# Optimization experiments

Measured on AMD Instinct MI355X. Metric: run time of the kernel, lower is better.

Reference implementation:

```python
import jax, jax.numpy as jnp
import numpy as np

K = 3
K2 = K * K
STRIDE, PAD, DIL = 1, 1, 1


def conv2d(x, w, b, stride, pad, dil):
    out = jax.lax.conv_general_dilated(
        x, w, (stride, stride), [(pad, pad), (pad, pad)],
        rhs_dilation=(dil, dil),
        dimension_numbers=("NCHW", "OIHW", "NCHW"))
    return out + b[None, :, None, None]


def deform_sample(img, py, px):
    """Bilinear sample with zero padding outside.
    img: [C,H,W]; py,px: [K2,Ho,Wo] float sample coords -> [C,K2,Ho,Wo]."""
    C, H, W = img.shape
    y0 = jnp.floor(py)
    x0 = jnp.floor(px)
    acc = jnp.zeros((C,) + py.shape, img.dtype)
    for dy in (0.0, 1.0):
        for dx in (0.0, 1.0):
            yi = y0 + dy
            xi = x0 + dx
            wgt = (1.0 - jnp.abs(py - yi)) * (1.0 - jnp.abs(px - xi))
            valid = (yi >= 0) & (yi < H) & (xi >= 0) & (xi < W)
            yc = jnp.clip(yi, 0, H - 1).astype(jnp.int32)
            xc = jnp.clip(xi, 0, W - 1).astype(jnp.int32)
            v = img[:, yc, xc]  # gather -> [C,K2,Ho,Wo]
            acc = acc + v * (wgt * valid)[None]
    return acc


def setup_inputs() -> dict:
    key = jax.random.key(0)
    k1, k2, k3, k4 = jax.random.split(key, 4)
    Cin, Cout = 64, 64
    x = jax.random.normal(k1, (4, Cin, 128, 128), jnp.float32)
    # small offset-conv weights so learned offsets stay in a few-pixel range
    w_off = jax.random.normal(k2, (3 * K2, Cin, K, K), jnp.float32) * 0.01
    b_off = jnp.zeros((3 * K2,), jnp.float32)
    # folded (BN-fused) deform conv weight/bias
    w = jax.random.normal(k3, (Cout, Cin, K, K), jnp.float32) * (1.0 / np.sqrt(Cin * K2))
    b = jax.random.normal(k4, (Cout,), jnp.float32) * 0.1
    return {"x": x, "w_off": w_off, "b_off": b_off, "w": w, "b": b}


def reference(x, w_off, b_off, w, b):
    N, C, H, W = x.shape
    # offset/mask conv -> chunk into (o1, o2, mask), cat offsets, sigmoid mask
    om = conv2d(x, w_off, b_off, STRIDE, PAD, DIL)  # [N, 27, Ho, Wo]
    o1, o2, m = jnp.split(om, 3, axis=1)
    offset = jnp.concatenate([o1, o2], axis=1)      # [N, 2*K2, Ho, Wo]
    mask = jax.nn.sigmoid(m)                        # [N, K2, Ho, Wo]
    Ho, Wo = offset.shape[2], offset.shape[3]
    # torchvision layout: per kernel tap (dy, dx) pairs
    off = offset.reshape(N, K2, 2, Ho, Wo)
    dy, dx = off[:, :, 0], off[:, :, 1]
    hk, wk = jnp.meshgrid(jnp.arange(K), jnp.arange(K), indexing="ij")
    base_y = ((jnp.arange(Ho) * STRIDE - PAD)[None, :, None]
              + (hk.reshape(K2) * DIL)[:, None, None])  # [K2,Ho,1]
    base_x = ((jnp.arange(Wo) * STRIDE - PAD)[None, None, :]
              + (wk.reshape(K2) * DIL)[:, None, None])  # [K2,1,Wo]
    py = base_y.astype(x.dtype) + dy                    # [N,K2,Ho,Wo]
    px = base_x.astype(x.dtype) + dx
    sampled = jax.vmap(deform_sample)(x, py, px)        # [N,C,K2,Ho,Wo]
    sampled = sampled * mask[:, None]
    out = jnp.einsum("ock,nckhw->nohw", w.reshape(w.shape[0], C, K2), sampled)
    out = out + b[None, :, None, None]
    return jax.nn.relu(out)
```

## Files before the change

kernel.cpp:

```cpp
#include <hip/hip_runtime.h>
#include <math.h>

#define N_ 4
#define C_ 64
#define H_ 128
#define W_ 128
#define HW_ (H_ * W_)
#define K2_ 9
#define COUT 64
#define CK 576
#define TP 16
#define NT 2
#define SST 584
#define GUARD 128
#define DEPTH 6
#define SLOTS 7

typedef __bf16 bf16x8 __attribute__((ext_vector_type(8)));
typedef __bf16 bf16x2 __attribute__((ext_vector_type(2)));
typedef float floatx4 __attribute__((ext_vector_type(4)));
typedef float floatx2 __attribute__((ext_vector_type(2)));
typedef unsigned uint2v __attribute__((ext_vector_type(2)));

__device__ __forceinline__ float bflo(unsigned u) {
    return __builtin_bit_cast(float, u << 16);
}
__device__ __forceinline__ float bfhi(unsigned u) {
    return __builtin_bit_cast(float, u & 0xffff0000u);
}

__global__ __launch_bounds__(256) void prep_kernel(const float* __restrict__ x,
                                                   const float* __restrict__ w,
                                                   const float* __restrict__ w_off,
                                                   __bf16* __restrict__ xT,
                                                   __bf16* __restrict__ w2,
                                                   __bf16* __restrict__ w_off2) {
    __shared__ float s_t[64][33];
    int t = threadIdx.x;
    int bx = blockIdx.x;
    int y = blockIdx.y, n = blockIdx.z;
    if (bx < 4) {
        int x0 = bx * 32;
        int c = t >> 2, seg = (t & 3) * 8;
        const float* src = x + (((size_t)n * C_ + c) * H_ + y) * W_ + x0 + seg;
        floatx4 v0 = *(const floatx4*)src;
        floatx4 v1 = *(const floatx4*)(src + 4);
#pragma unroll
        for (int j = 0; j < 4; ++j) { s_t[c][seg + j] = v0[j]; s_t[c][seg + 4 + j] = v1[j]; }
        __syncthreads();
        int xl = t >> 3, cb = (t & 7) * 8;
        bf16x8 o;
#pragma unroll
        for (int j = 0; j < 8; ++j) o[j] = (__bf16)s_t[cb + j][xl];
        *(bf16x8*)(xT + (((size_t)n * H_ + y) * W_ + x0 + xl) * C_ + cb) = o;
    } else {
        int linear = (n * 128 + y) * 256 + t;
        if (linear < COUT * CK) {
            int o = linear / CK, r = linear - o * CK;
            int k = r >> 6, c = r & 63;
            w2[linear] = (__bf16)w[(o * C_ + c) * K2_ + k];
        }
        if (linear < 32 * CK) {
            int o = linear / CK, r = linear - o * CK;
            int k = r >> 6, c = r & 63;
            w_off2[linear] = (o < 27) ? (__bf16)w_off[(o * C_ + c) * K2_ + k] : (__bf16)0.f;
        }
    }
}

__global__ __launch_bounds__(256) void fused_kernel(const __bf16* __restrict__ xT,
                                                    const __bf16* __restrict__ w2,
                                                    const __bf16* __restrict__ w_off2,
                                                    const float* __restrict__ b_off,
                                                    const float* __restrict__ b,
                                                    float* __restrict__ out) {
    __shared__ __align__(16) __bf16 s_x[NT][TP * SST];
    __shared__ float s_om[NT][2][32 * TP];
    __shared__ floatx4 s_w4[NT][K2_ * TP];
    __shared__ int s_pix[NT][K2_ * TP];

    int t = threadIdx.x;
    int pixbase = blockIdx.x * (TP * NT);
    int wo0 = pixbase & (W_ - 1);
    int ho  = (pixbase >> 7) & (H_ - 1);
    int n   = pixbase >> 14;
    const __bf16* xn = xT + (size_t)n * HW_ * C_;

    int lane = t & 63;
    int wv   = t >> 6;
    int half = lane >> 5;
    int li   = lane & 31;
    int q    = lane >> 4;
    int col  = lane & 15;

    {
        uint2v ua[18];
        int tl = wv >> 1;
        int rb = (wv & 1) * 36 + half;
#pragma unroll
        for (int j = 0; j < 18; ++j) {
            int r  = rb + 2 * j;
            int k  = r >> 3;
            int p0 = (r & 7) * 2;
            int kh = k / 3, kw = k - kh * 3;
            int y  = ho - 1 + kh;
            int yc = min(max(y, 0), H_ - 1);
            int xx = wo0 + 16 * tl + p0 - 1 + kw;
            int pix = yc * W_ + xx;
            ua[j] = *((const uint2v*)(xn + (ptrdiff_t)pix * C_) + li);
        }
#pragma unroll
        for (int j = 0; j < 18; ++j) {
            int r  = rb + 2 * j;
            int k  = r >> 3;
            int p0 = (r & 7) * 2;
            int kh = k / 3, kw = k - kh * 3;
            int y  = ho - 1 + kh;
            int xx = wo0 + 16 * tl + p0 - 1 + kw;
            bool vy = (unsigned)y < (unsigned)H_;
            int myxx = xx + (li >> 4);
            bool valid = vy && ((unsigned)myxx < (unsigned)W_);
            uint2v v = ua[j];
            v.x = valid ? v.x : 0u;
            v.y = valid ? v.y : 0u;
            int p = p0 + (li >> 4);
            *(uint2v*)&s_x[tl][p * SST + k * 64 + 4 * (li & 15)] = v;
        }
    }
    __syncthreads();

    {
        int r = wv >> 1;
        int h = wv & 1;
        const __bf16* ar = w_off2 + (size_t)(16 * r + col) * CK + h * 288 + q * 8;
        const __bf16* b0 = s_x[0] + col * SST + h * 288 + q * 8;
        const __bf16* b1 = s_x[1] + col * SST + h * 288 + q * 8;
        floatx4 acc0 = {0.f, 0.f, 0.f, 0.f}, acc1 = {0.f, 0.f, 0.f, 0.f};
#pragma unroll
        for (int it = 0; it < 9; ++it) {
            bf16x8 a   = *(const bf16x8*)(ar + 32 * it);
            bf16x8 bb0 = *(const bf16x8*)(b0 + 32 * it);
            bf16x8 bb1 = *(const bf16x8*)(b1 + 32 * it);
            acc0 = __builtin_amdgcn_mfma_f32_16x16x32_bf16(a, bb0, acc0, 0, 0, 0);
            acc1 = __builtin_amdgcn_mfma_f32_16x16x32_bf16(a, bb1, acc1, 0, 0, 0);
        }
#pragma unroll
        for (int rr = 0; rr < 4; ++rr) {
            s_om[0][h][(16 * r + q * 4 + rr) * TP + col] = acc0[rr];
            s_om[1][h][(16 * r + q * 4 + rr) * TP + col] = acc1[rr];
        }
    }
    __syncthreads();

#pragma unroll
    for (int it2 = 0; it2 < 2; ++it2) {
        int i = it2 * 256 + t;
        if (i < NT * K2_ * TP) {
            int tl = (i >= 144);
            int P  = i - 144 * tl;
            int k  = P >> 4;
            int pp = P & 15;
            float dy = s_om[tl][0][(2 * k) * TP + pp]     + s_om[tl][1][(2 * k) * TP + pp]     + b_off[2 * k];
            float dx = s_om[tl][0][(2 * k + 1) * TP + pp] + s_om[tl][1][(2 * k + 1) * TP + pp] + b_off[2 * k + 1];
            float mm = s_om[tl][0][(18 + k) * TP + pp]    + s_om[tl][1][(18 + k) * TP + pp]    + b_off[18 + k];
            float msk = 1.f / (1.f + expf(-mm));
            int kh = k / 3, kw = k - kh * 3;
            float py = (float)(ho - 1 + kh) + dy;
            float px = (float)(wo0 + 16 * tl + pp - 1 + kw) + dx;
            float yf = floorf(py), xf = floorf(px);
            float fy = py - yf, fx = px - xf;
            int y0 = (int)yf, x0 = (int)xf;
            float wy0 = ((unsigned)y0 < (unsigned)H_)       ? 1.f - fy : 0.f;
            float wy1 = ((unsigned)(y0 + 1) < (unsigned)H_) ? fy       : 0.f;
            float wx0 = ((unsigned)x0 < (unsigned)W_)       ? 1.f - fx : 0.f;
            float wx1 = ((unsigned)(x0 + 1) < (unsigned)W_) ? fx      : 0.f;
            int y0c = min(max(y0, 0), H_ - 2);
            int x0c = min(max(x0, 0), W_ - 2);
            float t0 = (y0 == y0c) ? wy0 : ((y0 + 1 == y0c) ? wy1 : 0.f);
            float t1 = (y0 == y0c) ? wy1 : ((y0 == y0c + 1) ? wy0 : 0.f);
            float u0 = (x0 == x0c) ? wx0 : ((x0 + 1 == x0c) ? wx1 : 0.f);
            float u1 = (x0 == x0c) ? wx1 : ((x0 == x0c + 1) ? wx0 : 0.f);
            floatx4 w4 = { t0 * u0 * msk, t0 * u1 * msk, t1 * u0 * msk, t1 * u1 * msk };
            s_w4[tl][P] = w4;
            s_pix[tl][P] = y0c * W_ + x0c;
        }
    }
    __syncthreads();

    {
        int Pb = wv * 36 + half;
        int pixv[36];
#pragma unroll
        for (int i = 0; i < 36; ++i) {
            int tl_ = (i >= 18);
            pixv[i] = s_pix[tl_][Pb + 2 * (i - 18 * tl_)];
        }
        unsigned buf[SLOTS][4];

#define ISSUE(gi)                                                                  \
        do {                                                                       \
            const __bf16* a0 = xn + (ptrdiff_t)pixv[(gi)] * C_ + 2 * li;           \
            const __bf16* a1 = a0 + W_ * C_;                                       \
            asm volatile("global_load_dword %0, %4, off\n\t"                       \
                         "global_load_dword %1, %4, off offset:128\n\t"            \
                         "global_load_dword %2, %5, off\n\t"                       \
                         "global_load_dword %3, %5, off offset:128"                \
                         : "=&v"(buf[(gi) % SLOTS][0]), "=&v"(buf[(gi) % SLOTS][1]),\
                           "=&v"(buf[(gi) % SLOTS][2]), "=&v"(buf[(gi) % SLOTS][3])\
                         : "v"(a0), "v"(a1));                                      \
        } while (0)

#define STEP(g, NW)                                                                \
        do {                                                                       \
            if ((g) + DEPTH < 36) ISSUE((g) + DEPTH);                              \
            int tl_ = ((g) >= 18);                                                 \
            int P_  = Pb + 2 * ((g) - 18 * tl_);                                   \
            floatx4 w4_ = s_w4[tl_][P_];                                           \
            asm volatile("s_waitcnt vmcnt(" #NW ")" ::: "memory");                 \
            __builtin_amdgcn_sched_barrier(0);                                     \
            float lo = w4_[0] * bflo(buf[(g) % SLOTS][0])                          \
                     + w4_[1] * bflo(buf[(g) % SLOTS][1])                          \
                     + w4_[2] * bflo(buf[(g) % SLOTS][2])                          \
                     + w4_[3] * bflo(buf[(g) % SLOTS][3]);                         \
            float hi = w4_[0] * bfhi(buf[(g) % SLOTS][0])                          \
                     + w4_[1] * bfhi(buf[(g) % SLOTS][1])                          \
                     + w4_[2] * bfhi(buf[(g) % SLOTS][2])                          \
                     + w4_[3] * bfhi(buf[(g) % SLOTS][3]);                         \
            floatx2 fv = {lo, hi};                                                 \
            bf16x2 bv = __builtin_convertvector(fv, bf16x2);                       \
            int k_ = P_ >> 4, p_ = P_ & 15;                                        \
            *(unsigned*)&s_x[tl_][p_ * SST + k_ * 64 + 2 * li] =                   \
                __builtin_bit_cast(unsigned, bv);                                  \
        } while (0)

        ISSUE(0); ISSUE(1); ISSUE(2); ISSUE(3); ISSUE(4); ISSUE(5);
        STEP(0, 24);  STEP(1, 24);  STEP(2, 24);  STEP(3, 24);  STEP(4, 24);
        STEP(5, 24);  STEP(6, 24);  STEP(7, 24);  STEP(8, 24);  STEP(9, 24);
        STEP(10, 24); STEP(11, 24); STEP(12, 24); STEP(13, 24); STEP(14, 24);
        STEP(15, 24); STEP(16, 24); STEP(17, 24); STEP(18, 24); STEP(19, 24);
        STEP(20, 24); STEP(21, 24); STEP(22, 24); STEP(23, 24); STEP(24, 24);
        STEP(25, 24); STEP(26, 24); STEP(27, 24); STEP(28, 24); STEP(29, 24);
        STEP(30, 20); STEP(31, 16); STEP(32, 12); STEP(33, 8);  STEP(34, 4);
        STEP(35, 0);
#undef STEP
#undef ISSUE
    }
    __syncthreads();

    {
        const __bf16* ar = w2 + (size_t)(16 * wv + col) * CK + q * 8;
        const __bf16* b0 = s_x[0] + col * SST + q * 8;
        const __bf16* b1 = s_x[1] + col * SST + q * 8;
        floatx4 acc0 = {0.f, 0.f, 0.f, 0.f}, acc1 = {0.f, 0.f, 0.f, 0.f};
        bf16x8 a_cur = *(const bf16x8*)ar;
#pragma unroll
        for (int it = 0; it < 18; ++it) {
            bf16x8 a_nxt;
            if (it < 17) a_nxt = *(const bf16x8*)(ar + 32 * (it + 1));
            bf16x8 bb0 = *(const bf16x8*)(b0 + 32 * it);
            bf16x8 bb1 = *(const bf16x8*)(b1 + 32 * it);
            acc0 = __builtin_amdgcn_mfma_f32_16x16x32_bf16(a_cur, bb0, acc0, 0, 0, 0);
            acc1 = __builtin_amdgcn_mfma_f32_16x16x32_bf16(a_cur, bb1, acc1, 0, 0, 0);
            a_cur = a_nxt;
        }
#pragma unroll
        for (int r = 0; r < 4; ++r) {
            int o = 16 * wv + q * 4 + r;
            float bias = b[o];
            float* ob = out + (((size_t)n * COUT + o) * H_ + ho) * W_ + wo0;
            ob[col]      = fmaxf(acc0[r] + bias, 0.f);
            ob[16 + col] = fmaxf(acc1[r] + bias, 0.f);
        }
    }
}

extern "C" void kernel_launch(void* const* d_in, const int* in_sizes, int n_in,
                              void* d_out, int out_size, void* d_ws, size_t ws_size,
                              hipStream_t stream) {
    const float* x     = (const float*)d_in[0];
    const float* w_off = (const float*)d_in[1];
    const float* b_off = (const float*)d_in[2];
    const float* w     = (const float*)d_in[3];
    const float* b     = (const float*)d_in[4];
    float* out = (float*)d_out;

    __bf16* xT     = (__bf16*)d_ws + GUARD;
    __bf16* w2     = xT + (size_t)N_ * HW_ * C_ + GUARD;
    __bf16* w_off2 = w2 + (size_t)COUT * CK;

    prep_kernel<<<dim3(5, 128, 4), 256, 0, stream>>>(x, w, w_off, xT, w2, w_off2);

    int nblocks = N_ * H_ * W_ / (TP * NT);
    fused_kernel<<<nblocks, 256, 0, stream>>>(xT, w2, w_off2, b_off, b, out);
}
```

Baseline: 119.8 us.

## Stage halo rows once in LDS instead of a replicated im2col tile for offset conv

The offset-conv input staging is replaced. Instead of building a 9x-replicated im2col tile per pixel, it loads 3 input rows by 34 pixels by 64 channels as 16-byte vectors into shared memory. The MFMA loop then indexes taps through row and column offsets. This cuts global loads, from 18 narrow loads per thread to 4 wide ones, and cuts LDS writes. The cost is a compile-time branch on h, and padded pixel strides chosen to limit bank conflicts.

```diff
diff --git a/kernel.cpp b/kernel.cpp
--- a/kernel.cpp
+++ b/kernel.cpp
@@ -15,12 +15,15 @@
 #define GUARD 128
 #define DEPTH 6
 #define SLOTS 7
+#define PXS 68
+#define RS  (34 * PXS)
 
 typedef __bf16 bf16x8 __attribute__((ext_vector_type(8)));
 typedef __bf16 bf16x2 __attribute__((ext_vector_type(2)));
 typedef float floatx4 __attribute__((ext_vector_type(4)));
 typedef float floatx2 __attribute__((ext_vector_type(2)));
 typedef unsigned uint2v __attribute__((ext_vector_type(2)));
+typedef unsigned uint4v __attribute__((ext_vector_type(4)));
 
 __device__ __forceinline__ float bflo(unsigned u) {
     return __builtin_bit_cast(float, u << 16);
@@ -78,6 +81,7 @@
     __shared__ float s_om[NT][2][32 * TP];
     __shared__ floatx4 s_w4[NT][K2_ * TP];
     __shared__ int s_pix[NT][K2_ * TP];
+    __bf16* s_row = &s_x[0][0];
 
     int t = threadIdx.x;
     int pixbase = blockIdx.x * (TP * NT);
@@ -94,37 +98,33 @@
     int col  = lane & 15;
 
     {
-        uint2v ua[18];
-        int tl = wv >> 1;
-        int rb = (wv & 1) * 36 + half;
-#pragma unroll
-        for (int j = 0; j < 18; ++j) {
-            int r  = rb + 2 * j;
-            int k  = r >> 3;
-            int p0 = (r & 7) * 2;
-            int kh = k / 3, kw = k - kh * 3;
-            int y  = ho - 1 + kh;
+        uint4v va[4];
+#pragma unroll
+        for (int it = 0; it < 4; ++it) {
+            int i  = it * 256 + t;
+            int s  = i & 7;
+            int pr = i >> 3;
+            int r  = pr / 34;
+            int p  = pr - r * 34;
+            int y  = ho - 1 + r;
             int yc = min(max(y, 0), H_ - 1);
-            int xx = wo0 + 16 * tl + p0 - 1 + kw;
-            int pix = yc * W_ + xx;
-            ua[j] = *((const uint2v*)(xn + (ptrdiff_t)pix * C_) + li);
-        }
-#pragma unroll
-        for (int j = 0; j < 18; ++j) {
-            int r  = rb + 2 * j;
-            int k  = r >> 3;
-            int p0 = (r & 7) * 2;
-            int kh = k / 3, kw = k - kh * 3;
-            int y  = ho - 1 + kh;
-            int xx = wo0 + 16 * tl + p0 - 1 + kw;
-            bool vy = (unsigned)y < (unsigned)H_;
-            int myxx = xx + (li >> 4);
-            bool valid = vy && ((unsigned)myxx < (unsigned)W_);
-            uint2v v = ua[j];
-            v.x = valid ? v.x : 0u;
-            v.y = valid ? v.y : 0u;
-            int p = p0 + (li >> 4);
-            *(uint2v*)&s_x[tl][p * SST + k * 64 + 4 * (li & 15)] = v;
+            int x  = wo0 - 1 + p;
+            const __bf16* ap = xn + (ptrdiff_t)(yc * W_ + x) * C_ + s * 8;
+            va[it] = *(const uint4v*)ap;
+        }
+#pragma unroll
+        for (int it = 0; it < 4; ++it) {
+            int i  = it * 256 + t;
+            int s  = i & 7;
+            int pr = i >> 3;
+            int r  = pr / 34;
+            int p  = pr - r * 34;
+            int y  = ho - 1 + r;
+            int x  = wo0 - 1 + p;
+            bool valid = ((unsigned)y < (unsigned)H_) && ((unsigned)x < (unsigned)W_);
+            uint4v v = va[it];
+            if (!valid) v = (uint4v){0u, 0u, 0u, 0u};
+            if (i < 3 * 34 * 8) *(uint4v*)&s_row[r * RS + p * PXS + s * 8] = v;
         }
     }
     __syncthreads();
@@ -132,18 +132,31 @@
     {
         int r = wv >> 1;
         int h = wv & 1;
-        const __bf16* ar = w_off2 + (size_t)(16 * r + col) * CK + h * 288 + q * 8;
-        const __bf16* b0 = s_x[0] + col * SST + h * 288 + q * 8;
-        const __bf16* b1 = s_x[1] + col * SST + h * 288 + q * 8;
+        const __bf16* ar  = w_off2 + (size_t)(16 * r + col) * CK + h * 288 + q * 8;
+        const __bf16* rb0 = s_row + col * PXS + q * 8;
+        const __bf16* rb1 = rb0 + 16 * PXS;
         floatx4 acc0 = {0.f, 0.f, 0.f, 0.f}, acc1 = {0.f, 0.f, 0.f, 0.f};
-#pragma unroll
-        for (int it = 0; it < 9; ++it) {
-            bf16x8 a   = *(const bf16x8*)(ar + 32 * it);
-            bf16x8 bb0 = *(const bf16x8*)(b0 + 32 * it);
-            bf16x8 bb1 = *(const bf16x8*)(b1 + 32 * it);
-            acc0 = __builtin_amdgcn_mfma_f32_16x16x32_bf16(a, bb0, acc0, 0, 0, 0);
-            acc1 = __builtin_amdgcn_mfma_f32_16x16x32_bf16(a, bb1, acc1, 0, 0, 0);
-        }
+#define BSTEP(j, KBASE)                                                              \
+        {                                                                            \
+            const int K_  = (KBASE) + (j) * 32;                                      \
+            const int kk  = K_ >> 6;                                                 \
+            const int ch  = (K_ >> 5) & 1;                                           \
+            const int kh  = kk / 3, kw = kk - kh * 3;                                \
+            const int off = kh * RS + kw * PXS + ch * 32;                            \
+            bf16x8 a  = *(const bf16x8*)(ar + 32 * (j));                             \
+            bf16x8 b0 = *(const bf16x8*)(rb0 + off);                                 \
+            bf16x8 b1 = *(const bf16x8*)(rb1 + off);                                 \
+            acc0 = __builtin_amdgcn_mfma_f32_16x16x32_bf16(a, b0, acc0, 0, 0, 0);    \
+            acc1 = __builtin_amdgcn_mfma_f32_16x16x32_bf16(a, b1, acc1, 0, 0, 0);    \
+        }
+        if (h == 0) {
+            BSTEP(0, 0) BSTEP(1, 0) BSTEP(2, 0) BSTEP(3, 0) BSTEP(4, 0)
+            BSTEP(5, 0) BSTEP(6, 0) BSTEP(7, 0) BSTEP(8, 0)
+        } else {
+            BSTEP(0, 288) BSTEP(1, 288) BSTEP(2, 288) BSTEP(3, 288) BSTEP(4, 288)
+            BSTEP(5, 288) BSTEP(6, 288) BSTEP(7, 288) BSTEP(8, 288)
+        }
+#undef BSTEP
 #pragma unroll
         for (int rr = 0; rr < 4; ++rr) {
             s_om[0][h][(16 * r + q * 4 + rr) * TP + col] = acc0[rr];
```

New measurement: 122.4 us. 2.1% more time.
